# Performance work log

Hardware: AMD Instinct MI355X
Metric: run time of the kernel (lower is better)

Reference implementation:

```python
import jax, jax.numpy as jnp
import numpy as np

INPUT_MIN, INPUT_MAX = -1.0, 1.0
GRID = 16

def setup_inputs() -> dict:
    key = jax.random.key(0)
    k1, k2 = jax.random.split(key)
    B, D, O, P = 8192, 768, 16, 384
    x = jax.random.normal(k1, (B, D), dtype=jnp.float32)
    # pair coeffs stacked: [P, O, G, G, 3]; torch init: c[...,0]=0, c[...,1:3] ~ N(0, 0.1)
    coeffs = jax.random.normal(k2, (P, O, GRID, GRID, 3), dtype=jnp.float32) * 0.1
    coeffs = coeffs.at[..., 0].set(0.0)
    bias = jnp.zeros((O,), dtype=jnp.float32)
    return {"x": x, "coeffs": coeffs, "bias": bias}

def reference(x, coeffs, bias):
    # x: [B, D] with D even; coeffs: [P, O, G, G, 3]; bias: [O]
    P = coeffs.shape[0]
    x_norm = jnp.clip((x - INPUT_MIN) / (INPUT_MAX - INPUT_MIN), 0.0, 1.0 - 1e-6)
    a = x_norm[:, 0::2]  # [B, P]
    b = x_norm[:, 1::2]  # [B, P]
    idx_a = jnp.clip((a * GRID).astype(jnp.int32), 0, GRID - 1)
    idx_b = jnp.clip((b * GRID).astype(jnp.int32), 0, GRID - 1)
    p_idx = jnp.arange(P, dtype=jnp.int32)[None, :]  # [1, P]
    # advanced-index gather -> c: [B, P, O, 3]
    c = coeffs[p_idx, :, idx_a, idx_b]
    feats = jnp.stack([jnp.ones_like(a), a, b], axis=-1)  # [B, P, 3]
    out = jnp.einsum('bpoc,bpc->bo', c, feats)  # sum over pairs and coeff triple
    return out + bias
```

## Files before the change

### kernel.cpp

```cpp
#include <hip/hip_runtime.h>
#include <hip/hip_fp16.h>


#define D_N    768
#define O_N    16
#define P_N    384
#define GRID_N 16
#define CELLS  256
#define NCHUNK 8
#define P_CH   (P_N / NCHUNK)
#define BT     16
#define CELLB  128
#define ABO_STRIDE 52

static __device__ __forceinline__ float clipnorm(float v) {
    const float CLIPMAX = (float)(1.0 - 1e-6);
    return fminf(fmaxf((v + 1.0f) * 0.5f, 0.0f), CLIPMAX);
}

static __device__ __forceinline__ float h2f(unsigned short u) {
    __half_raw r; r.x = u;
    return __half2float(__half(r));
}

__global__ void build_ct16_kernel(const float* __restrict__ src,
                                  ushort4* __restrict__ dst) {
    int t = blockIdx.x * 256 + threadIdx.x;
    int o    = t & 15;
    int cell = (t >> 4) & 255;
    int p    = t >> 12;
    const float* s = src + ((size_t)(p * O_N + o) * CELLS + cell) * 3;
    ushort4 v;
    v.x = __half_raw(__float2half_rn(s[0])).x;
    v.y = __half_raw(__float2half_rn(s[1])).x;
    v.z = __half_raw(__float2half_rn(s[2])).x;
    v.w = 0;
    dst[t] = v;
}

__global__ __launch_bounds__(256) void spline_stage1_kernel(
        const float* __restrict__ x, const ushort4* __restrict__ ct,
        float* __restrict__ part, int n_bo) {
    __shared__ float4 abo[BT * ABO_STRIDE];

    int chunk = blockIdx.x & (NCHUNK - 1);
    int btile = blockIdx.x >> 3;
    int b0 = btile * BT;

    for (int i = threadIdx.x; i < BT * P_CH; i += 256) {
        int bl = i / P_CH;
        int pl = i - bl * P_CH;
        const float* xp = x + (size_t)(b0 + bl) * D_N + chunk * (2 * P_CH) + 2 * pl;
        float an = clipnorm(xp[0]);
        float bn = clipnorm(xp[1]);
        int ia = (int)(an * 16.0f);
        int ib = (int)(bn * 16.0f);
        int off = (ia * GRID_N + ib) * CELLB;
        abo[bl * ABO_STRIDE + pl] = make_float4(an, bn, __int_as_float(off), 0.0f);
    }
    __syncthreads();

    int o  = threadIdx.x & 15;
    int bl = threadIdx.x >> 4;
    const char* cbase = (const char*)ct
        + (size_t)chunk * P_CH * CELLS * CELLB + o * 8;
    const float4* ab = &abo[bl * ABO_STRIDE];

    float acc = 0.0f;
#pragma unroll 4
    for (int pl = 0; pl < P_CH; ++pl) {
        float4 v = ab[pl];
        int off = __float_as_int(v.z);
        ushort4 c = *(const ushort4*)(cbase + (size_t)pl * (CELLS * CELLB) + off);
        acc += h2f(c.x);
        acc = fmaf(h2f(c.y), v.x, acc);
        acc = fmaf(h2f(c.z), v.y, acc);
    }
    part[(size_t)chunk * n_bo + (size_t)(b0 + bl) * O_N + o] = acc;
}

__global__ void spline_stage2_kernel(const float* __restrict__ part,
                                     const float* __restrict__ bias,
                                     float* __restrict__ out, int n_bo) {
    int t = blockIdx.x * 256 + threadIdx.x;
    if (t >= n_bo) return;
    float s = bias[t & 15];
#pragma unroll
    for (int c = 0; c < NCHUNK; ++c) s += part[(size_t)c * n_bo + t];
    out[t] = s;
}

__global__ void spline_naive_kernel(const float* __restrict__ x,
                                    const float* __restrict__ coeffs,
                                    const float* __restrict__ bias,
                                    float* __restrict__ out, int Btot) {
    int t = blockIdx.x * 256 + threadIdx.x;
    if (t >= Btot * O_N) return;
    int o = t & 15;
    int b = t >> 4;
    const float* xrow = x + (size_t)b * D_N;
    float acc = bias[o];
    for (int p = 0; p < P_N; ++p) {
        float an = clipnorm(xrow[2 * p]);
        float bn = clipnorm(xrow[2 * p + 1]);
        int ia = (int)(an * 16.0f);
        int ib = (int)(bn * 16.0f);
        const float* cp = coeffs + ((size_t)(p * O_N + o) * CELLS
                                    + ia * GRID_N + ib) * 3;
        acc += cp[0];
        acc = fmaf(cp[1], an, acc);
        acc = fmaf(cp[2], bn, acc);
    }
    out[t] = acc;
}

extern "C" void kernel_launch(void* const* d_in, const int* in_sizes, int n_in,
                              void* d_out, int out_size, void* d_ws, size_t ws_size,
                              hipStream_t stream) {
    const float* x      = (const float*)d_in[0];
    const float* coeffs = (const float*)d_in[1];
    const float* bias   = (const float*)d_in[2];
    float* out = (float*)d_out;

    int B = in_sizes[0] / D_N;
    int n_bo = B * O_N;
    size_t ct_bytes   = (size_t)P_N * CELLS * CELLB;
    size_t part_bytes = (size_t)NCHUNK * n_bo * sizeof(float);

    if (ws_size >= ct_bytes + part_bytes && (B % BT) == 0) {
        ushort4* ct = (ushort4*)d_ws;
        float* part = (float*)((char*)d_ws + ct_bytes);
        build_ct16_kernel<<<(P_N * CELLS * O_N) / 256, 256, 0, stream>>>(coeffs, ct);
        spline_stage1_kernel<<<(B / BT) * NCHUNK, 256, 0, stream>>>(x, ct, part, n_bo);
        spline_stage2_kernel<<<(n_bo + 255) / 256, 256, 0, stream>>>(part, bias, out, n_bo);
    } else {
        spline_naive_kernel<<<(B * O_N + 255) / 256, 256, 0, stream>>>(x, coeffs, bias, out, B);
    }
}
```

Before: 112.0 us.

## Stage coefficient transpose through LDS and split stage1 accumulator chain

The coefficient fp16 repack kernel now loads each pair's contiguous fp32 block into shared memory with coalesced float4 reads, then writes the transposed ushort4 layout. The goal is to replace the old strided 12-byte gathers from global memory. The stage1 loop is also unrolled by pairs into two independent accumulators, which shortens the FMA dependency chain and puts two gathers in flight at once. This costs a padded ~24KB LDS tile per block and adds a slight change to floating-point summation order.

```diff
diff --git a/kernel.cpp b/kernel.cpp
--- a/kernel.cpp
+++ b/kernel.cpp
@@ -23,19 +23,36 @@
     return __half2float(__half(r));
 }
 
-__global__ void build_ct16_kernel(const float* __restrict__ src,
-                                  ushort4* __restrict__ dst) {
-    int t = blockIdx.x * 256 + threadIdx.x;
-    int o    = t & 15;
-    int cell = (t >> 4) & 255;
-    int p    = t >> 12;
-    const float* s = src + ((size_t)(p * O_N + o) * CELLS + cell) * 3;
-    ushort4 v;
-    v.x = __half_raw(__float2half_rn(s[0])).x;
-    v.y = __half_raw(__float2half_rn(s[1])).x;
-    v.z = __half_raw(__float2half_rn(s[2])).x;
-    v.w = 0;
-    dst[t] = v;
+__global__ __launch_bounds__(256) void build_ct16_v2_kernel(
+        const float* __restrict__ src, ushort4* __restrict__ dst) {
+    __shared__ float4 lds4[8 * 193];
+
+    int p  = blockIdx.x >> 1;
+    int oh = blockIdx.x & 1;
+
+    const float4* s4 = (const float4*)src + ((size_t)(p * O_N + oh * 8) * 192);
+    for (int g = threadIdx.x; g < 1536; g += 256) {
+        int o = g / 192;
+        int q = g - o * 192;
+        lds4[o * 193 + q] = s4[g];
+    }
+    __syncthreads();
+
+    const float* ldsf = (const float*)lds4;
+    ushort4* d = dst + (size_t)p * (CELLS * O_N) + oh * 8;
+#pragma unroll
+    for (int k = 0; k < 8; ++k) {
+        int j    = k * 256 + threadIdx.x;
+        int o8   = j & 7;
+        int cell = j >> 3;
+        int base = o8 * 772 + cell * 3;
+        ushort4 v;
+        v.x = __half_raw(__float2half_rn(ldsf[base + 0])).x;
+        v.y = __half_raw(__float2half_rn(ldsf[base + 1])).x;
+        v.z = __half_raw(__float2half_rn(ldsf[base + 2])).x;
+        v.w = 0;
+        d[(size_t)cell * O_N + o8] = v;
+    }
 }
 
 __global__ __launch_bounds__(256) void spline_stage1_kernel(
@@ -66,17 +83,23 @@
         + (size_t)chunk * P_CH * CELLS * CELLB + o * 8;
     const float4* ab = &abo[bl * ABO_STRIDE];
 
-    float acc = 0.0f;
+    float acc0 = 0.0f, acc1 = 0.0f;
 #pragma unroll 4
-    for (int pl = 0; pl < P_CH; ++pl) {
-        float4 v = ab[pl];
-        int off = __float_as_int(v.z);
-        ushort4 c = *(const ushort4*)(cbase + (size_t)pl * (CELLS * CELLB) + off);
-        acc += h2f(c.x);
-        acc = fmaf(h2f(c.y), v.x, acc);
-        acc = fmaf(h2f(c.z), v.y, acc);
+    for (int pl = 0; pl < P_CH; pl += 2) {
+        float4 va = ab[pl];
+        float4 vb = ab[pl + 1];
+        int offa = __float_as_int(va.z);
+        int offb = __float_as_int(vb.z);
+        ushort4 ca = *(const ushort4*)(cbase + (size_t)pl * (CELLS * CELLB) + offa);
+        ushort4 cb2 = *(const ushort4*)(cbase + (size_t)(pl + 1) * (CELLS * CELLB) + offb);
+        acc0 += h2f(ca.x);
+        acc0 = fmaf(h2f(ca.y), va.x, acc0);
+        acc0 = fmaf(h2f(ca.z), va.y, acc0);
+        acc1 += h2f(cb2.x);
+        acc1 = fmaf(h2f(cb2.y), vb.x, acc1);
+        acc1 = fmaf(h2f(cb2.z), vb.y, acc1);
     }
-    part[(size_t)chunk * n_bo + (size_t)(b0 + bl) * O_N + o] = acc;
+    part[(size_t)chunk * n_bo + (size_t)(b0 + bl) * O_N + o] = acc0 + acc1;
 }
 
 __global__ void spline_stage2_kernel(const float* __restrict__ part,
@@ -130,7 +153,7 @@
     if (ws_size >= ct_bytes + part_bytes && (B % BT) == 0) {
         ushort4* ct = (ushort4*)d_ws;
         float* part = (float*)((char*)d_ws + ct_bytes);
-        build_ct16_kernel<<<(P_N * CELLS * O_N) / 256, 256, 0, stream>>>(coeffs, ct);
+        build_ct16_v2_kernel<<<P_N * 2, 256, 0, stream>>>(coeffs, ct);
         spline_stage1_kernel<<<(B / BT) * NCHUNK, 256, 0, stream>>>(x, ct, part, n_bo);
         spline_stage2_kernel<<<(n_bo + 255) / 256, 256, 0, stream>>>(part, bias, out, n_bo);
     } else {
```

New measurement: 109.4 us. -2.3%, faster.
